# Performance work log

Measured on AMD Instinct MI355X. Metric: run time of the kernel, lower is better.

The kernel has to match this reference:

```python
import jax, jax.numpy as jnp
import numpy as np
from jax import lax

K = 3          # kernel size
STRIDE = 1
PAD = 1
DIL = 1

def setup_inputs() -> dict:
    key = jax.random.key(0)
    k1, k2 = jax.random.split(key)
    N, C, H, W = 8, 256, 56, 56
    Cw = 32                      # weight channels = C // share_planes (share=8)
    L = H * W                    # stride 1, pad 1 -> same spatial size
    inp = jax.random.normal(k1, (N, C, H, W), dtype=jnp.float32)
    weight = jax.random.normal(k2, (N, Cw, K * K, L), dtype=jnp.float32)
    return {"input": inp, "weight": weight}

def reference(input, weight):
    N, C, H, W = input.shape
    _, Cw, KK, L = weight.shape
    share = C // Cw
    # Extract KxK patches (zero padding). Output: [N, C*K*K, Ho, Wo],
    # feature dim ordered channel-outermost, matching torch unfold.
    patches = lax.conv_general_dilated_patches(
        input, filter_shape=(K, K), window_strides=(STRIDE, STRIDE),
        padding=[(PAD, PAD), (PAD, PAD)], rhs_dilation=(DIL, DIL))
    Ho, Wo = patches.shape[2], patches.shape[3]
    # [N, Cw, share, K*K, L]
    patches = patches.reshape(N, Cw, share, KK, Ho * Wo)
    # broadcast weight over share channels, reduce over kernel taps
    out = jnp.einsum('ngskl,ngkl->ngsl', patches, weight)
    return out.reshape(N, C, Ho, Wo)
```

## Files before the change

kernel.cpp:

```cpp
#include <hip/hip_runtime.h>


#define HH 56
#define WW 56
#define LL 3136
#define CW 32
#define SHARE 8
#define CC 256
#define NN 8

__global__ __launch_bounds__(256) void agg_kernel(const float* __restrict__ in,
                                                  const float* __restrict__ wt,
                                                  float* __restrict__ out) {
    const int l = blockIdx.x * 256 + threadIdx.x;
    const int g = blockIdx.y;
    const int n = blockIdx.z;
    if (l >= LL) return;
    const int h = l / WW;
    const int w = l - h * WW;

    const float* wp = wt + (((size_t)n * CW + g) * 9) * LL + l;
    float w9[9];
#pragma unroll
    for (int kk = 0; kk < 9; ++kk) w9[kk] = wp[(size_t)kk * LL];

    int off[9];
    bool val[9];
#pragma unroll
    for (int kk = 0; kk < 9; ++kk) {
        const int hh = h + kk / 3 - 1;
        const int ww = w + kk % 3 - 1;
        val[kk] = ((unsigned)hh < (unsigned)HH) && ((unsigned)ww < (unsigned)WW);
        off[kk] = hh * WW + ww;
    }

    const int c0 = g * SHARE;
    const float* ip = in + ((size_t)n * CC + c0) * LL;
    float* op = out + ((size_t)n * CC + c0) * LL;
#pragma unroll
    for (int s = 0; s < SHARE; ++s) {
        float acc = 0.f;
#pragma unroll
        for (int kk = 0; kk < 9; ++kk) {
            const float v = val[kk] ? ip[(size_t)s * LL + off[kk]] : 0.f;
            acc = fmaf(v, w9[kk], acc);
        }
        op[(size_t)s * LL + l] = acc;
    }
}

extern "C" void kernel_launch(void* const* d_in, const int* in_sizes, int n_in,
                              void* d_out, int out_size, void* d_ws, size_t ws_size,
                              hipStream_t stream) {
    const float* in = (const float*)d_in[0];
    const float* wt = (const float*)d_in[1];
    float* out = (float*)d_out;
    dim3 grid((LL + 255) / 256, CW, NN);
    agg_kernel<<<grid, 256, 0, stream>>>(in, wt, out);
}
```

Baseline: 21.72 us.

## Rewrite aggregation with per-wave channel tiles, float4 loads and shuffle-based halo exchange

Each block now covers an 8-row band of one (n, group). Each of its 8 wavefronts handles one of the group's 8 channels, and each lane computes 8 consecutive output pixels. Input rows are read with float4 loads, and vertical and horizontal neighbors come from wavefront shuffles rather than repeated scattered global loads. Halo rows at band edges are loaded explicitly. The block index is swizzled across 8 chunks, apparently to spread work across XCDs. The aim is fewer redundant loads and vectorized memory access. In exchange, each wave loads the weights separately, so weight reads rise from one per group to one per channel, and 8 of the 64 lanes sit idle.

```diff
diff --git a/kernel.cpp b/kernel.cpp
--- a/kernel.cpp
+++ b/kernel.cpp
@@ -5,47 +5,87 @@
 #define WW 56
 #define LL 3136
 #define CW 32
-#define SHARE 8
 #define CC 256
 #define NN 8
+#define NWG (NN * CW * 7)
+#define CHUNK (NWG / 8)
 
-__global__ __launch_bounds__(256) void agg_kernel(const float* __restrict__ in,
+__global__ __launch_bounds__(512) void agg_kernel(const float* __restrict__ in,
                                                   const float* __restrict__ wt,
                                                   float* __restrict__ out) {
-    const int l = blockIdx.x * 256 + threadIdx.x;
-    const int g = blockIdx.y;
-    const int n = blockIdx.z;
-    if (l >= LL) return;
-    const int h = l / WW;
-    const int w = l - h * WW;
+    const unsigned t    = threadIdx.x;
+    const unsigned wid  = t >> 6;
+    const unsigned lane = t & 63u;
+    const unsigned bp   = blockIdx.x;
+    const unsigned b    = (bp & 7u) * CHUNK + (bp >> 3);
+    const unsigned band = b % 7u;
+    const unsigned ng   = b / 7u;
+    const unsigned g    = ng & 31u;
+    const unsigned n    = ng >> 5;
 
-    const float* wp = wt + (((size_t)n * CW + g) * 9) * LL + l;
-    float w9[9];
+    const unsigned rq = (lane < 56u) ? lane : 55u;
+    const unsigned r  = rq / 7u;
+    const unsigned q  = rq - r * 7u;
+    const unsigned h  = band * 8u + r;
+    const unsigned w8 = q * 8u;
+    const unsigned l  = h * WW + w8;
+
+    const unsigned c  = g * 8u + wid;
+    const float* ip = in + ((size_t)n * CC + c) * LL;
+
+    const float4 cA = *(const float4*)(ip + l);
+    const float4 cB = *(const float4*)(ip + l + 4);
+    float4 hmA = make_float4(0.f,0.f,0.f,0.f), hmB = hmA;
+    float4 hpA = hmA, hpB = hmA;
+    if (r == 0u && h > 0u)      { hmA = *(const float4*)(ip + l - WW);
+                                  hmB = *(const float4*)(ip + l - WW + 4); }
+    if (r == 7u && h < HH - 1u) { hpA = *(const float4*)(ip + l + WW);
+                                  hpB = *(const float4*)(ip + l + WW + 4); }
+
+    float cv[8] = {cA.x, cA.y, cA.z, cA.w, cB.x, cB.y, cB.z, cB.w};
+    float hm[8] = {hmA.x, hmA.y, hmA.z, hmA.w, hmB.x, hmB.y, hmB.z, hmB.w};
+    float hp[8] = {hpA.x, hpA.y, hpA.z, hpA.w, hpB.x, hpB.y, hpB.z, hpB.w};
+
+    float cm[8], cp[8];
 #pragma unroll
-    for (int kk = 0; kk < 9; ++kk) w9[kk] = wp[(size_t)kk * LL];
-
-    int off[9];
-    bool val[9];
-#pragma unroll
-    for (int kk = 0; kk < 9; ++kk) {
-        const int hh = h + kk / 3 - 1;
-        const int ww = w + kk % 3 - 1;
-        val[kk] = ((unsigned)hh < (unsigned)HH) && ((unsigned)ww < (unsigned)WW);
-        off[kk] = hh * WW + ww;
+    for (int i = 0; i < 8; ++i) {
+        const float su = __shfl_up(cv[i], 7);
+        const float sd = __shfl_down(cv[i], 7);
+        cm[i] = (r == 0u) ? hm[i] : su;
+        cp[i] = (r == 7u) ? hp[i] : sd;
     }
 
-    const int c0 = g * SHARE;
-    const float* ip = in + ((size_t)n * CC + c0) * LL;
-    float* op = out + ((size_t)n * CC + c0) * LL;
+    float lm = __shfl_up(cm[7], 1), lc = __shfl_up(cv[7], 1), lp = __shfl_up(cp[7], 1);
+    float em = __shfl_down(cm[0], 1), ec = __shfl_down(cv[0], 1), ep = __shfl_down(cp[0], 1);
+    if (q == 0u) { lm = 0.f; lc = 0.f; lp = 0.f; }
+    if (q == 6u) { em = 0.f; ec = 0.f; ep = 0.f; }
+
+    float win[3][10];
 #pragma unroll
-    for (int s = 0; s < SHARE; ++s) {
-        float acc = 0.f;
+    for (int i = 0; i < 8; ++i) { win[0][i+1] = cm[i]; win[1][i+1] = cv[i]; win[2][i+1] = cp[i]; }
+    win[0][0] = lm; win[1][0] = lc; win[2][0] = lp;
+    win[0][9] = em; win[1][9] = ec; win[2][9] = ep;
+
+    const float* wp = wt + (((size_t)n * CW + g) * 9u) * LL + l;
+    float acc[8] = {0.f, 0.f, 0.f, 0.f, 0.f, 0.f, 0.f, 0.f};
 #pragma unroll
-        for (int kk = 0; kk < 9; ++kk) {
-            const float v = val[kk] ? ip[(size_t)s * LL + off[kk]] : 0.f;
-            acc = fmaf(v, w9[kk], acc);
+    for (int dr = 0; dr < 3; ++dr) {
+#pragma unroll
+        for (int dw = 0; dw < 3; ++dw) {
+            const int k = dr * 3 + dw;
+            const float4 wA = *(const float4*)(wp + (size_t)k * LL);
+            const float4 wB = *(const float4*)(wp + (size_t)k * LL + 4);
+            const float wv8[8] = {wA.x, wA.y, wA.z, wA.w, wB.x, wB.y, wB.z, wB.w};
+#pragma unroll
+            for (int e = 0; e < 8; ++e)
+                acc[e] = fmaf(win[dr][e + dw], wv8[e], acc[e]);
         }
-        op[(size_t)s * LL + l] = acc;
+    }
+
+    if (lane < 56u) {
+        float* op = out + ((size_t)n * CC + c) * LL + l;
+        *(float4*)op       = make_float4(acc[0], acc[1], acc[2], acc[3]);
+        *(float4*)(op + 4) = make_float4(acc[4], acc[5], acc[6], acc[7]);
     }
 }
 
@@ -55,6 +95,5 @@
     const float* in = (const float*)d_in[0];
     const float* wt = (const float*)d_in[1];
     float* out = (float*)d_out;
-    dim3 grid((LL + 255) / 256, CW, NN);
-    agg_kernel<<<grid, 256, 0, stream>>>(in, wt, out);
+    agg_kernel<<<dim3(NWG), dim3(512), 0, stream>>>(in, wt, out);
 }
```

New measurement: 22.43 us. +3.3%, slower.
